# Kernel optimization log

Measured on AMD Instinct MI355X. Metric: run time of the kernel, lower is better.

Reference implementation:

```python
import jax, jax.numpy as jnp
import numpy as np

N, D, IN, HID, OUT, E = 20000, 8, 64, 128, 64, 100000
EPS = 1e-5


def _bn(h, g, b):
    # training-mode BatchNorm1d: biased batch variance, eps=1e-5
    m = h.mean(axis=0)
    v = jnp.mean((h - m) ** 2, axis=0)
    return (h - m) * jax.lax.rsqrt(v + EPS) * g + b


def setup_inputs() -> dict:
    key = jax.random.key(0)
    ks = jax.random.split(key, 12)
    x = jax.random.normal(ks[0], (N, IN), dtype=jnp.float32)
    node_ts = jax.random.uniform(ks[1], (N,), dtype=jnp.float32)
    neighbor_idx = jax.random.randint(ks[2], (N, D), 0, N, dtype=jnp.int32)
    neighbor_ts = jax.random.uniform(ks[3], (N, D), dtype=jnp.float32)
    target = jax.random.randint(ks[4], (2, E), 0, N, dtype=jnp.int32)
    neg_pairs = jax.random.randint(ks[5], (2, E), 0, N, dtype=jnp.int32)
    W1 = jax.random.normal(ks[6], (IN, HID), dtype=jnp.float32) * (1.0 / np.sqrt(IN))
    b1 = jnp.zeros((HID,), jnp.float32)
    g1 = jnp.ones((HID,), jnp.float32)
    be1 = jnp.zeros((HID,), jnp.float32)
    W2 = jax.random.normal(ks[7], (HID, OUT), dtype=jnp.float32) * (1.0 / np.sqrt(HID))
    b2 = jnp.zeros((OUT,), jnp.float32)
    g2 = jnp.ones((OUT,), jnp.float32)
    be2 = jnp.zeros((OUT,), jnp.float32)
    Wd = jax.random.normal(ks[8], (OUT, 1), dtype=jnp.float32) * (1.0 / np.sqrt(OUT))
    bd = jnp.zeros((1,), jnp.float32)
    return {"x": x, "node_ts": node_ts, "neighbor_idx": neighbor_idx,
            "neighbor_ts": neighbor_ts, "target": target, "neg_pairs": neg_pairs,
            "W1": W1, "b1": b1, "g1": g1, "be1": be1,
            "W2": W2, "b2": b2, "g2": g2, "be2": be2, "Wd": Wd, "bd": bd}


def reference(x, node_ts, neighbor_idx, neighbor_ts, target, neg_pairs,
              W1, b1, g1, be1, W2, b2, g2, be2, Wd, bd):
    n = jnp.arange(N, dtype=neighbor_idx.dtype)
    # ---- level-2 queries: every node at its own timestamp ----
    # children = D temporal-neighbor slots + self (self always valid, ts=node_ts)
    c_idx = jnp.concatenate([neighbor_idx, n[:, None]], axis=1)          # [N, D+1]
    c_ts = jnp.concatenate([neighbor_ts, node_ts[:, None]], axis=1)      # [N, D+1]
    mask2 = jnp.concatenate([neighbor_ts <= node_ts[:, None],
                             jnp.ones((N, 1), bool)], axis=1)            # [N, D+1]
    # ---- level-1 queries: each (child node, child ts) pair ----
    ci = c_idx.reshape(-1)                                               # [M]
    cts = c_ts.reshape(-1)
    gc_idx = jnp.concatenate([neighbor_idx[ci], ci[:, None]], axis=1)    # [M, D+1]
    mask1 = jnp.concatenate([neighbor_ts[ci] <= cts[:, None],
                             jnp.ones((ci.shape[0], 1), bool)], axis=1)
    # ---- layer 0: raw features of grandchildren ----
    h0 = x[gc_idx]                                                       # [M, D+1, IN]
    m1 = mask1.astype(x.dtype)
    agg1 = jnp.einsum('mk,mkf->mf', m1, h0) / m1.sum(1, keepdims=True)   # masked mean
    h1 = jax.nn.relu(_bn(agg1 @ W1 + b1, g1, be1))                       # [M, HID]
    h1 = h1.reshape(N, D + 1, HID)
    # ---- layer 2 aggregation over temporal children ----
    m2 = mask2.astype(x.dtype)
    agg2 = jnp.einsum('nk,nkf->nf', m2, h1) / m2.sum(1, keepdims=True)
    embs = jax.nn.relu(_bn(agg2 @ W2 + b2, g2, be2))                     # [N, OUT]
    # ---- HadNet link decoder + BCEWithLogits ----
    pos = (embs[target[0]] * embs[target[1]]) @ Wd + bd                  # [E, 1]
    neg = (embs[neg_pairs[0]] * embs[neg_pairs[1]]) @ Wd + bd            # [E, 1]
    preds = jnp.concatenate([pos, neg], axis=0)[:, 0]                    # [2E]
    labels = jnp.concatenate([jnp.ones((E,), x.dtype), jnp.zeros((E,), x.dtype)])
    loss = jnp.mean(jnp.maximum(preds, 0.0) - preds * labels
                    + jnp.log1p(jnp.exp(-jnp.abs(preds))))
    return loss
```

## Files before the change

### kernel.cpp

```cpp
#include <hip/hip_runtime.h>
#include <math.h>

constexpr int kN = 20000;
constexpr int kD = 8;
constexpr int kE = 100000;
constexpr int kM = kN * 9;
constexpr int kTiles1 = kM / 16;
constexpr int kTilesN = kN / 16;
constexpr float kEps = 1e-5f;

constexpr int S_SUM1 = 0, S_SQ1 = 128, S_SUM2 = 256, S_SQ2 = 320;

constexpr size_t OFF_M     = 0;
constexpr size_t OFF_PRE2  = 23040000;
constexpr size_t OFF_STATS = 28160000;
constexpr size_t OFF_CNT   = OFF_STATS + 1536;
constexpr size_t OFF_RI    = OFF_CNT + 720000;

typedef short short8 __attribute__((ext_vector_type(8)));
typedef float floatx4 __attribute__((ext_vector_type(4)));

__device__ __forceinline__ unsigned f2bf(float f) {
  unsigned u = __float_as_uint(f);
  u += 0x7fffu + ((u >> 16) & 1u);
  return u >> 16;
}

__global__ __launch_bounds__(256) void k0_prefix(
    const float* __restrict__ x, const float* __restrict__ node_ts,
    const int* __restrict__ nidx, const float* __restrict__ nts,
    unsigned short* __restrict__ M, int* __restrict__ rowinfo,
    float* __restrict__ cntf)
{
  int c = blockIdx.x * 4 + (threadIdx.x >> 6);
  const int lane = threadIdx.x & 63;
  c = __builtin_amdgcn_readfirstlane(c);

  float ts[8]; int id[8];
#pragma unroll
  for (int j = 0; j < kD; ++j) { ts[j] = nts[c * kD + j]; id[j] = nidx[c * kD + j]; }

#define CSWAP(A, B)                                                   \
  { float ta = ts[A], tb = ts[B]; int ia = id[A], ib = id[B];         \
    bool sw = tb < ta;                                                \
    ts[A] = sw ? tb : ta; ts[B] = sw ? ta : tb;                       \
    id[A] = sw ? ib : ia; id[B] = sw ? ia : ib; }
  CSWAP(0, 1) CSWAP(2, 3) CSWAP(0, 2) CSWAP(1, 3) CSWAP(1, 2)
  CSWAP(4, 5) CSWAP(6, 7) CSWAP(4, 6) CSWAP(5, 7) CSWAP(5, 6)
  CSWAP(0, 4) CSWAP(1, 5) CSWAP(2, 6) CSWAP(3, 7)
  CSWAP(2, 4) CSWAP(3, 5)
  CSWAP(1, 2) CSWAP(3, 4) CSWAP(5, 6)
#undef CSWAP

  float s = x[c * 64 + lane];
  unsigned short* mp = M + (size_t)c * 9 * 64 + lane;
  mp[0] = (unsigned short)f2bf(s);
#pragma unroll
  for (int r = 1; r <= kD; ++r) {
    s += x[id[r - 1] * 64 + lane];
    mp[r * 64] = (unsigned short)f2bf(s / (float)(r + 1));
  }

  const int m = blockIdx.x * 256 + threadIdx.x;
  if (m < kM) {
    const int n = (int)((unsigned)m / 9u);
    const int slot = m - n * 9;
    int cc; float t;
    if (slot < kD) { cc = nidx[n * kD + slot]; t = nts[n * kD + slot]; }
    else           { cc = n;                   t = node_ts[n]; }
    int rank = 0;
#pragma unroll
    for (int j = 0; j < kD; ++j) rank += (nts[cc * kD + j] <= t) ? 1 : 0;
    rowinfo[m] = cc * 9 + rank;
    atomicAdd(&cntf[cc * 9 + rank], 1.0f);
  }
}

__global__ __launch_bounds__(256, 3) void k1_stats(
    const unsigned short* __restrict__ M, const float* __restrict__ cntf,
    const float* __restrict__ W1, const float* __restrict__ b1,
    float* __restrict__ stats)
{
  __shared__ unsigned short W1T[128 * 72];
  __shared__ float redS[256][8];
  __shared__ float redQ[256][8];

  const int tid = threadIdx.x;
  const int lane = tid & 63;
  const int wave = tid >> 6;
  const int l15 = lane & 15;
  const int q = lane >> 4;

  for (int i = tid; i < 8192; i += 256) {
    int n = i >> 6, k = i & 63;
    W1T[n * 72 + k] = (unsigned short)f2bf(W1[k * 128 + n]);
  }
  __syncthreads();

  short8 bf[8][2];
#pragma unroll
  for (int cc = 0; cc < 8; ++cc)
#pragma unroll
    for (int s = 0; s < 2; ++s)
      bf[cc][s] = *(const short8*)&W1T[(cc * 16 + l15) * 72 + q * 8 + s * 32];

  float b1c[8];
#pragma unroll
  for (int cc = 0; cc < 8; ++cc) b1c[cc] = b1[cc * 16 + l15];

  float sum8[8], sq8[8];
#pragma unroll
  for (int cc = 0; cc < 8; ++cc) { sum8[cc] = 0.f; sq8[cc] = 0.f; }

  const int gw = blockIdx.x * 4 + wave;
  const int nw = gridDim.x * 4;

  for (int t = gw; t < kTiles1; t += nw) {
    const unsigned short* mp = M + (size_t)(t * 16 + l15) * 64;
    short8 af0 = *(const short8*)(mp + q * 8);
    short8 af1 = *(const short8*)(mp + 32 + q * 8);
    float c4[4];
#pragma unroll
    for (int i = 0; i < 4; ++i) c4[i] = cntf[t * 16 + q * 4 + i];

    floatx4 acc[8];
#pragma unroll
    for (int cc = 0; cc < 8; ++cc) {
      acc[cc] = (floatx4){0.f, 0.f, 0.f, 0.f};
      acc[cc] = __builtin_amdgcn_mfma_f32_16x16x32_bf16(af0, bf[cc][0], acc[cc], 0, 0, 0);
      acc[cc] = __builtin_amdgcn_mfma_f32_16x16x32_bf16(af1, bf[cc][1], acc[cc], 0, 0, 0);
    }
#pragma unroll
    for (int cc = 0; cc < 8; ++cc) {
#pragma unroll
      for (int i = 0; i < 4; ++i) {
        float v = acc[cc][i] + b1c[cc];
        sum8[cc] += c4[i] * v;
        sq8[cc]  += c4[i] * v * v;
      }
    }
  }

  __syncthreads();
#pragma unroll
  for (int cc = 0; cc < 8; ++cc) { redS[tid][cc] = sum8[cc]; redQ[tid][cc] = sq8[cc]; }
  __syncthreads();
  if (tid < 128) {
    int cc = tid >> 4, r15 = tid & 15;
    float s = 0.f, qq = 0.f;
#pragma unroll
    for (int w = 0; w < 4; ++w)
#pragma unroll
      for (int p = 0; p < 4; ++p) {
        int T = w * 64 + p * 16 + r15;
        s += redS[T][cc]; qq += redQ[T][cc];
      }
    atomicAdd(&stats[S_SUM1 + tid], s);
    atomicAdd(&stats[S_SQ1 + tid], qq);
  }
}

__global__ __launch_bounds__(256, 2) void k3_fused(
    const unsigned short* __restrict__ M, const int* __restrict__ rowinfo,
    const float* __restrict__ node_ts, const float* __restrict__ nts,
    const float* __restrict__ stats_in, const float* __restrict__ g1,
    const float* __restrict__ be1, const float* __restrict__ W1,
    const float* __restrict__ b1, const float* __restrict__ W2,
    const float* __restrict__ b2, float* __restrict__ stats_out,
    float* __restrict__ pre2)
{
  __shared__ __attribute__((aligned(16))) unsigned short W1T[128 * 72];
  __shared__ __attribute__((aligned(16))) unsigned short W2T[64 * 136];
  __shared__ __attribute__((aligned(16))) unsigned short sm[144 * 132];
  __shared__ __attribute__((aligned(16))) unsigned short aggT[16 * 136];
  __shared__ float sc1[128], sh1[128];
  __shared__ float wlds[144];
  __shared__ float winv[16];

  const int tid = threadIdx.x;
  const int lane = tid & 63;
  const int wave = tid >> 6;
  const int l15 = lane & 15;
  const int q = lane >> 4;

  for (int i = tid; i < 8192; i += 256) {
    int n = i >> 6, k = i & 63;
    W1T[n * 72 + k] = (unsigned short)f2bf(W1[k * 128 + n]);
  }
  for (int i = tid; i < 8192; i += 256) {
    int n = i >> 7, k = i & 127;
    W2T[n * 136 + k] = (unsigned short)f2bf(W2[k * 64 + n]);
  }
  if (tid < 128) {
    float mean = stats_in[S_SUM1 + tid] * (1.f / kM);
    float var  = stats_in[S_SQ1 + tid] * (1.f / kM) - mean * mean;
    float s    = g1[tid] * rsqrtf(var + kEps);
    sc1[tid] = s; sh1[tid] = be1[tid] - mean * s;
  }
  __syncthreads();

  short8 bf[8][2];
  float b1c[8], scc[8], shc[8];
#pragma unroll
  for (int cc = 0; cc < 8; ++cc) {
    int col = cc * 16 + l15;
#pragma unroll
    for (int s = 0; s < 2; ++s)
      bf[cc][s] = *(const short8*)&W1T[col * 72 + q * 8 + s * 32];
    b1c[cc] = b1[col]; scc[cc] = sc1[col]; shc[cc] = sh1[col];
  }
  short8 bfr2[4];
#pragma unroll
  for (int s = 0; s < 4; ++s)
    bfr2[s] = *(const short8*)&W2T[(wave * 16 + l15) * 136 + q * 8 + s * 32];
  const float b2w = b2[wave * 16 + l15];

  float sumS = 0.f, sumQ = 0.f;

  for (int tb = blockIdx.x; tb < kTilesN; tb += gridDim.x) {
    const int node0 = tb * 16;
    const int row0 = tb * 144;

    if (tid < 144) {
      int ln = tid / 9;
      int slot = tid - ln * 9;
      int nn = node0 + ln;
      float w = 1.f;
      if (slot < kD) w = (nts[nn * kD + slot] <= node_ts[nn]) ? 1.f : 0.f;
      wlds[tid] = w;
    }
    __syncthreads();
    if (tid < 16) {
      float swv = 0.f;
#pragma unroll
      for (int r = 0; r < 9; ++r) swv += wlds[tid * 9 + r];
      winv[tid] = 1.f / swv;
    }

    for (int tl = wave; tl < 9; tl += 4) {
      const int ri = rowinfo[row0 + tl * 16 + l15];
      const unsigned short* mp = M + (size_t)ri * 64;
      short8 af0 = *(const short8*)(mp + q * 8);
      short8 af1 = *(const short8*)(mp + 32 + q * 8);
      floatx4 acc[8];
#pragma unroll
      for (int cc = 0; cc < 8; ++cc) {
        acc[cc] = (floatx4){0.f, 0.f, 0.f, 0.f};
        acc[cc] = __builtin_amdgcn_mfma_f32_16x16x32_bf16(af0, bf[cc][0], acc[cc], 0, 0, 0);
        acc[cc] = __builtin_amdgcn_mfma_f32_16x16x32_bf16(af1, bf[cc][1], acc[cc], 0, 0, 0);
      }
#pragma unroll
      for (int cc = 0; cc < 8; ++cc) {
        int col = cc * 16 + l15;
#pragma unroll
        for (int i = 0; i < 4; ++i) {
          float v = acc[cc][i] + b1c[cc];
          float val = fmaxf(fmaf(v, scc[cc], shc[cc]), 0.f);
          int rl = tl * 16 + q * 4 + i;
          val *= wlds[rl];
          sm[rl * 132 + col] = (unsigned short)f2bf(val);
        }
      }
    }
    __syncthreads();

#pragma unroll
    for (int k = 0; k < 4; ++k) {
      int it = tid + k * 256;
      int nd = it >> 6, cp = it & 63;
      float s0 = 0.f, s1 = 0.f;
#pragma unroll
      for (int r = 0; r < 9; ++r) {
        unsigned u = *(const unsigned*)&sm[(nd * 9 + r) * 132 + cp * 2];
        s0 += __uint_as_float(u << 16);
        s1 += __uint_as_float(u & 0xffff0000u);
      }
      float iv = winv[nd];
      *(unsigned*)&aggT[nd * 136 + cp * 2] = f2bf(s0 * iv) | (f2bf(s1 * iv) << 16);
    }
    __syncthreads();

    short8 af2[4];
#pragma unroll
    for (int s = 0; s < 4; ++s)
      af2[s] = *(const short8*)&aggT[l15 * 136 + q * 8 + s * 32];
    floatx4 acc2 = (floatx4){0.f, 0.f, 0.f, 0.f};
#pragma unroll
    for (int s = 0; s < 4; ++s)
      acc2 = __builtin_amdgcn_mfma_f32_16x16x32_bf16(af2[s], bfr2[s], acc2, 0, 0, 0);
#pragma unroll
    for (int i = 0; i < 4; ++i) {
      float v = acc2[i] + b2w;
      int nrow = node0 + q * 4 + i;
      pre2[(size_t)nrow * 64 + wave * 16 + l15] = v;
      sumS += v; sumQ += v * v;
    }
  }

  sumS += __shfl_xor(sumS, 16); sumS += __shfl_xor(sumS, 32);
  sumQ += __shfl_xor(sumQ, 16); sumQ += __shfl_xor(sumQ, 32);
  if (lane < 16) {
    atomicAdd(&stats_out[S_SUM2 + wave * 16 + lane], sumS);
    atomicAdd(&stats_out[S_SQ2 + wave * 16 + lane], sumQ);
  }
}

__global__ __launch_bounds__(256) void k6_loss(
    const float* __restrict__ pre2, const float* __restrict__ stats,
    const float* __restrict__ g2, const float* __restrict__ be2,
    const float* __restrict__ Wd, const int* __restrict__ tgt,
    const int* __restrict__ neg, const float* __restrict__ bd,
    float* __restrict__ out)
{
  __shared__ float scl[64], shl[64], wdl[64];
  __shared__ float redl[256];
  const int tid = threadIdx.x;
  if (tid < 64) {
    float mean = stats[S_SUM2 + tid] * (1.f / kN);
    float var  = stats[S_SQ2 + tid] * (1.f / kN) - mean * mean;
    float s    = g2[tid] * rsqrtf(var + kEps);
    scl[tid] = s; shl[tid] = be2[tid] - mean * s; wdl[tid] = Wd[tid];
  }
  __syncthreads();

  const int tq = tid & 15;
  const int qb = tid >> 4;
  const int c0 = tq * 4;
  const float4 sc4 = {scl[c0], scl[c0 + 1], scl[c0 + 2], scl[c0 + 3]};
  const float4 sh4 = {shl[c0], shl[c0 + 1], shl[c0 + 2], shl[c0 + 3]};
  const float4 wd4 = {wdl[c0], wdl[c0 + 1], wdl[c0 + 2], wdl[c0 + 3]};
  const float bd0 = bd[0];

  float lsum = 0.f;
  const int e0 = blockIdx.x * 128 + qb * 8;
#pragma unroll
  for (int it = 0; it < 8; ++it) {
    int e = e0 + it;
    if (e < 2 * kE) {
      int i, j; float lab;
      if (e < kE) { i = tgt[e];      j = tgt[kE + e]; lab = 1.f; }
      else        { i = neg[e - kE]; j = neg[e];      lab = 0.f; }
      float4 a = *(const float4*)(pre2 + (size_t)i * 64 + c0);
      float4 b = *(const float4*)(pre2 + (size_t)j * 64 + c0);
      float eix = fmaxf(fmaf(a.x, sc4.x, sh4.x), 0.f) * wd4.x;
      float eiy = fmaxf(fmaf(a.y, sc4.y, sh4.y), 0.f) * wd4.y;
      float eiz = fmaxf(fmaf(a.z, sc4.z, sh4.z), 0.f) * wd4.z;
      float eiw = fmaxf(fmaf(a.w, sc4.w, sh4.w), 0.f) * wd4.w;
      float ejx = fmaxf(fmaf(b.x, sc4.x, sh4.x), 0.f);
      float ejy = fmaxf(fmaf(b.y, sc4.y, sh4.y), 0.f);
      float ejz = fmaxf(fmaf(b.z, sc4.z, sh4.z), 0.f);
      float ejw = fmaxf(fmaf(b.w, sc4.w, sh4.w), 0.f);
      float p = eix * ejx + eiy * ejy + eiz * ejz + eiw * ejw;
      p += __shfl_xor(p, 1); p += __shfl_xor(p, 2);
      p += __shfl_xor(p, 4); p += __shfl_xor(p, 8);
      p += bd0;
      float l = fmaxf(p, 0.f) - p * lab + log1pf(expf(-fabsf(p)));
      if (tq == 0) lsum += l;
    }
  }
  redl[tid] = lsum;
  __syncthreads();
  for (int s = 128; s > 0; s >>= 1) {
    if (tid < s) redl[tid] += redl[tid + s];
    __syncthreads();
  }
  if (tid == 0) atomicAdd(out, redl[0] * (1.f / (2 * kE)));
}

extern "C" void kernel_launch(void* const* d_in, const int* in_sizes, int n_in,
                              void* d_out, int out_size, void* d_ws, size_t ws_size,
                              hipStream_t stream) {
  (void)in_sizes; (void)n_in; (void)out_size; (void)ws_size;
  const float* x       = (const float*)d_in[0];
  const float* node_ts = (const float*)d_in[1];
  const int*   nidx    = (const int*)d_in[2];
  const float* nts     = (const float*)d_in[3];
  const int*   tgt     = (const int*)d_in[4];
  const int*   neg     = (const int*)d_in[5];
  const float* W1      = (const float*)d_in[6];
  const float* b1      = (const float*)d_in[7];
  const float* g1      = (const float*)d_in[8];
  const float* be1     = (const float*)d_in[9];
  const float* W2      = (const float*)d_in[10];
  const float* b2      = (const float*)d_in[11];
  const float* g2      = (const float*)d_in[12];
  const float* be2     = (const float*)d_in[13];
  const float* Wd      = (const float*)d_in[14];
  const float* bd      = (const float*)d_in[15];

  char* ws = (char*)d_ws;
  unsigned short* Mbuf = (unsigned short*)(ws + OFF_M);
  float* pre2  = (float*)(ws + OFF_PRE2);
  float* stats = (float*)(ws + OFF_STATS);
  float* cntf  = (float*)(ws + OFF_CNT);
  int*   rinfo = (int*)(ws + OFF_RI);
  float* out   = (float*)d_out;

  hipMemsetAsync(stats, 0, 1536 + 720000, stream);
  hipMemsetAsync(out, 0, sizeof(float), stream);

  k0_prefix<<<kN / 4, 256, 0, stream>>>(x, node_ts, nidx, nts, Mbuf, rinfo, cntf);
  k1_stats<<<704, 256, 0, stream>>>(Mbuf, cntf, W1, b1, stats);
  k3_fused<<<512, 256, 0, stream>>>(Mbuf, rinfo, node_ts, nts, stats, g1, be1,
                                    W1, b1, W2, b2, stats, pre2);
  k6_loss<<<(2 * kE + 127) / 128, 256, 0, stream>>>(pre2, stats, g2, be2, Wd,
                                                    tgt, neg, bd, out);
}
```

Baseline: 207.1 us.

## Fuse all stages into one persistent kernel with software grid barriers

Merges the four kernel launches into one persistent kernel of 512 blocks. Stages are separated by atomic-counter grid barriers, and the W1/W2 bf16 transposes are staged once per block instead of once per kernel. It also adds a pass that writes post-BN2 embeddings as bf16, so the loss stage gathers half the bytes and skips the per-edge BN math. This removes launch gaps and redundant weight setup, but adds five grid-wide spin barriers, relies on all 512 blocks being co-resident, and lowers embedding precision to bf16.

Measured after the change: 440.4 us. 2.13x slower.

```diff
diff --git a/kernel.cpp b/kernel.cpp
--- a/kernel.cpp
+++ b/kernel.cpp
@@ -8,14 +8,18 @@
 constexpr int kTiles1 = kM / 16;
 constexpr int kTilesN = kN / 16;
 constexpr float kEps = 1e-5f;
+constexpr int kGrid = 512;
+constexpr int kThreads = 256;
 
 constexpr int S_SUM1 = 0, S_SQ1 = 128, S_SUM2 = 256, S_SQ2 = 320;
 
 constexpr size_t OFF_M     = 0;
 constexpr size_t OFF_PRE2  = 23040000;
-constexpr size_t OFF_STATS = 28160000;
-constexpr size_t OFF_CNT   = OFF_STATS + 1536;
-constexpr size_t OFF_RI    = OFF_CNT + 720000;
+constexpr size_t OFF_EMBS  = 28160000;
+constexpr size_t OFF_STATS = 30720000;
+constexpr size_t OFF_CNT   = 30721536;
+constexpr size_t OFF_RI    = 31441536;
+constexpr size_t OFF_BAR   = 32161536;
 
 typedef short short8 __attribute__((ext_vector_type(8)));
 typedef float floatx4 __attribute__((ext_vector_type(4)));
@@ -26,43 +30,96 @@
   return u >> 16;
 }
 
-__global__ __launch_bounds__(256) void k0_prefix(
+__device__ __forceinline__ void grid_bar(int* bar, int target) {
+  __syncthreads();
+  if (threadIdx.x == 0) {
+    __threadfence();
+    __hip_atomic_fetch_add(bar, 1, __ATOMIC_RELEASE, __HIP_MEMORY_SCOPE_AGENT);
+    while (__hip_atomic_load(bar, __ATOMIC_RELAXED, __HIP_MEMORY_SCOPE_AGENT) < target)
+      __builtin_amdgcn_s_sleep(2);
+    __threadfence();
+  }
+  __syncthreads();
+}
+
+constexpr int kLdsBytes = 43008;
+
+__global__ __launch_bounds__(kThreads, 2) void k_all(
     const float* __restrict__ x, const float* __restrict__ node_ts,
     const int* __restrict__ nidx, const float* __restrict__ nts,
-    unsigned short* __restrict__ M, int* __restrict__ rowinfo,
-    float* __restrict__ cntf)
+    const int* __restrict__ tgt, const int* __restrict__ neg,
+    const float* __restrict__ W1, const float* __restrict__ b1,
+    const float* __restrict__ g1, const float* __restrict__ be1,
+    const float* __restrict__ W2, const float* __restrict__ b2,
+    const float* __restrict__ g2, const float* __restrict__ be2,
+    const float* __restrict__ Wd, const float* __restrict__ bd,
+    unsigned short* __restrict__ Mb, float* __restrict__ pre2,
+    unsigned short* __restrict__ embs, float* __restrict__ stats,
+    float* __restrict__ cntf, int* __restrict__ rowinfo,
+    int* bar, float* out)
 {
-  int c = blockIdx.x * 4 + (threadIdx.x >> 6);
-  const int lane = threadIdx.x & 63;
-  c = __builtin_amdgcn_readfirstlane(c);
-
-  float ts[8]; int id[8];
-#pragma unroll
-  for (int j = 0; j < kD; ++j) { ts[j] = nts[c * kD + j]; id[j] = nidx[c * kD + j]; }
-
+  __shared__ __attribute__((aligned(16))) char ldsb[kLdsBytes];
+
+  const int tid = threadIdx.x;
+  const int lane = tid & 63;
+  const int wave = tid >> 6;
+  const int l15 = lane & 15;
+  const int q = lane >> 4;
+  const int gw = blockIdx.x * 4 + wave;
+
+  unsigned short* W1T = (unsigned short*)ldsb;
+  unsigned short* W2T = (unsigned short*)(ldsb + 18432);
+
+  for (int i = tid; i < 8192; i += 256) {
+    int nn = i >> 6, k = i & 63;
+    W1T[nn * 72 + k] = (unsigned short)f2bf(W1[k * 128 + nn]);
+  }
+  for (int i = tid; i < 8192; i += 256) {
+    int nn = i >> 7, k = i & 127;
+    W2T[nn * 136 + k] = (unsigned short)f2bf(W2[k * 64 + nn]);
+  }
+  if (blockIdx.x == 0 && tid == 0) *out = 0.f;
+  __syncthreads();
+
+  short8 bf[8][2];
+  float b1c[8];
+#pragma unroll
+  for (int cc = 0; cc < 8; ++cc) {
+    int col = cc * 16 + l15;
+#pragma unroll
+    for (int s = 0; s < 2; ++s)
+      bf[cc][s] = *(const short8*)&W1T[col * 72 + q * 8 + s * 32];
+    b1c[cc] = b1[col];
+  }
+
+  grid_bar(bar, 1 * kGrid);
+
+  for (int c0 = gw; c0 < kN; c0 += kGrid * 4) {
+    const int c = __builtin_amdgcn_readfirstlane(c0);
+    float ts[8]; int id[8];
+#pragma unroll
+    for (int j = 0; j < kD; ++j) { ts[j] = nts[c * kD + j]; id[j] = nidx[c * kD + j]; }
 #define CSWAP(A, B)                                                   \
-  { float ta = ts[A], tb = ts[B]; int ia = id[A], ib = id[B];         \
-    bool sw = tb < ta;                                                \
-    ts[A] = sw ? tb : ta; ts[B] = sw ? ta : tb;                       \
-    id[A] = sw ? ib : ia; id[B] = sw ? ia : ib; }
-  CSWAP(0, 1) CSWAP(2, 3) CSWAP(0, 2) CSWAP(1, 3) CSWAP(1, 2)
-  CSWAP(4, 5) CSWAP(6, 7) CSWAP(4, 6) CSWAP(5, 7) CSWAP(5, 6)
-  CSWAP(0, 4) CSWAP(1, 5) CSWAP(2, 6) CSWAP(3, 7)
-  CSWAP(2, 4) CSWAP(3, 5)
-  CSWAP(1, 2) CSWAP(3, 4) CSWAP(5, 6)
+    { float ta = ts[A], tb = ts[B]; int ia = id[A], ib = id[B];       \
+      bool sw = tb < ta;                                              \
+      ts[A] = sw ? tb : ta; ts[B] = sw ? ta : tb;                     \
+      id[A] = sw ? ib : ia; id[B] = sw ? ia : ib; }
+    CSWAP(0, 1) CSWAP(2, 3) CSWAP(0, 2) CSWAP(1, 3) CSWAP(1, 2)
+    CSWAP(4, 5) CSWAP(6, 7) CSWAP(4, 6) CSWAP(5, 7) CSWAP(5, 6)
+    CSWAP(0, 4) CSWAP(1, 5) CSWAP(2, 6) CSWAP(3, 7)
+    CSWAP(2, 4) CSWAP(3, 5)
+    CSWAP(1, 2) CSWAP(3, 4) CSWAP(5, 6)
 #undef CSWAP
-
-  float s = x[c * 64 + lane];
-  unsigned short* mp = M + (size_t)c * 9 * 64 + lane;
-  mp[0] = (unsigned short)f2bf(s);
-#pragma unroll
-  for (int r = 1; r <= kD; ++r) {
-    s += x[id[r - 1] * 64 + lane];
-    mp[r * 64] = (unsigned short)f2bf(s / (float)(r + 1));
-  }
-
-  const int m = blockIdx.x * 256 + threadIdx.x;
-  if (m < kM) {
+    float s = x[c * 64 + lane];
+    unsigned short* mp = Mb + (size_t)c * 9 * 64 + lane;
+    mp[0] = (unsigned short)f2bf(s);
+#pragma unroll
+    for (int r = 1; r <= kD; ++r) {
+      s += x[id[r - 1] * 64 + lane];
+      mp[r * 64] = (unsigned short)f2bf(s / (float)(r + 1));
+    }
+  }
+  for (int m = blockIdx.x * 256 + tid; m < kM; m += kGrid * 256) {
     const int n = (int)((unsigned)m / 9u);
     const int slot = m - n * 9;
     int cc; float t;
@@ -74,174 +131,22 @@
     rowinfo[m] = cc * 9 + rank;
     atomicAdd(&cntf[cc * 9 + rank], 1.0f);
   }
-}
-
-__global__ __launch_bounds__(256, 3) void k1_stats(
-    const unsigned short* __restrict__ M, const float* __restrict__ cntf,
-    const float* __restrict__ W1, const float* __restrict__ b1,
-    float* __restrict__ stats)
-{
-  __shared__ unsigned short W1T[128 * 72];
-  __shared__ float redS[256][8];
-  __shared__ float redQ[256][8];
-
-  const int tid = threadIdx.x;
-  const int lane = tid & 63;
-  const int wave = tid >> 6;
-  const int l15 = lane & 15;
-  const int q = lane >> 4;
-
-  for (int i = tid; i < 8192; i += 256) {
-    int n = i >> 6, k = i & 63;
-    W1T[n * 72 + k] = (unsigned short)f2bf(W1[k * 128 + n]);
-  }
-  __syncthreads();
-
-  short8 bf[8][2];
-#pragma unroll
-  for (int cc = 0; cc < 8; ++cc)
-#pragma unroll
-    for (int s = 0; s < 2; ++s)
-      bf[cc][s] = *(const short8*)&W1T[(cc * 16 + l15) * 72 + q * 8 + s * 32];
-
-  float b1c[8];
-#pragma unroll
-  for (int cc = 0; cc < 8; ++cc) b1c[cc] = b1[cc * 16 + l15];
-
-  float sum8[8], sq8[8];
-#pragma unroll
-  for (int cc = 0; cc < 8; ++cc) { sum8[cc] = 0.f; sq8[cc] = 0.f; }
-
-  const int gw = blockIdx.x * 4 + wave;
-  const int nw = gridDim.x * 4;
-
-  for (int t = gw; t < kTiles1; t += nw) {
-    const unsigned short* mp = M + (size_t)(t * 16 + l15) * 64;
-    short8 af0 = *(const short8*)(mp + q * 8);
-    short8 af1 = *(const short8*)(mp + 32 + q * 8);
-    float c4[4];
-#pragma unroll
-    for (int i = 0; i < 4; ++i) c4[i] = cntf[t * 16 + q * 4 + i];
-
-    floatx4 acc[8];
-#pragma unroll
-    for (int cc = 0; cc < 8; ++cc) {
-      acc[cc] = (floatx4){0.f, 0.f, 0.f, 0.f};
-      acc[cc] = __builtin_amdgcn_mfma_f32_16x16x32_bf16(af0, bf[cc][0], acc[cc], 0, 0, 0);
-      acc[cc] = __builtin_amdgcn_mfma_f32_16x16x32_bf16(af1, bf[cc][1], acc[cc], 0, 0, 0);
-    }
-#pragma unroll
-    for (int cc = 0; cc < 8; ++cc) {
-#pragma unroll
-      for (int i = 0; i < 4; ++i) {
-        float v = acc[cc][i] + b1c[cc];
-        sum8[cc] += c4[i] * v;
-        sq8[cc]  += c4[i] * v * v;
-      }
-    }
-  }
-
-  __syncthreads();
-#pragma unroll
-  for (int cc = 0; cc < 8; ++cc) { redS[tid][cc] = sum8[cc]; redQ[tid][cc] = sq8[cc]; }
-  __syncthreads();
-  if (tid < 128) {
-    int cc = tid >> 4, r15 = tid & 15;
-    float s = 0.f, qq = 0.f;
-#pragma unroll
-    for (int w = 0; w < 4; ++w)
-#pragma unroll
-      for (int p = 0; p < 4; ++p) {
-        int T = w * 64 + p * 16 + r15;
-        s += redS[T][cc]; qq += redQ[T][cc];
-      }
-    atomicAdd(&stats[S_SUM1 + tid], s);
-    atomicAdd(&stats[S_SQ1 + tid], qq);
-  }
-}
-
-__global__ __launch_bounds__(256, 2) void k3_fused(
-    const unsigned short* __restrict__ M, const int* __restrict__ rowinfo,
-    const float* __restrict__ node_ts, const float* __restrict__ nts,
-    const float* __restrict__ stats_in, const float* __restrict__ g1,
-    const float* __restrict__ be1, const float* __restrict__ W1,
-    const float* __restrict__ b1, const float* __restrict__ W2,
-    const float* __restrict__ b2, float* __restrict__ stats_out,
-    float* __restrict__ pre2)
-{
-  __shared__ __attribute__((aligned(16))) unsigned short W1T[128 * 72];
-  __shared__ __attribute__((aligned(16))) unsigned short W2T[64 * 136];
-  __shared__ __attribute__((aligned(16))) unsigned short sm[144 * 132];
-  __shared__ __attribute__((aligned(16))) unsigned short aggT[16 * 136];
-  __shared__ float sc1[128], sh1[128];
-  __shared__ float wlds[144];
-  __shared__ float winv[16];
-
-  const int tid = threadIdx.x;
-  const int lane = tid & 63;
-  const int wave = tid >> 6;
-  const int l15 = lane & 15;
-  const int q = lane >> 4;
-
-  for (int i = tid; i < 8192; i += 256) {
-    int n = i >> 6, k = i & 63;
-    W1T[n * 72 + k] = (unsigned short)f2bf(W1[k * 128 + n]);
-  }
-  for (int i = tid; i < 8192; i += 256) {
-    int n = i >> 7, k = i & 127;
-    W2T[n * 136 + k] = (unsigned short)f2bf(W2[k * 64 + n]);
-  }
-  if (tid < 128) {
-    float mean = stats_in[S_SUM1 + tid] * (1.f / kM);
-    float var  = stats_in[S_SQ1 + tid] * (1.f / kM) - mean * mean;
-    float s    = g1[tid] * rsqrtf(var + kEps);
-    sc1[tid] = s; sh1[tid] = be1[tid] - mean * s;
-  }
-  __syncthreads();
-
-  short8 bf[8][2];
-  float b1c[8], scc[8], shc[8];
-#pragma unroll
-  for (int cc = 0; cc < 8; ++cc) {
-    int col = cc * 16 + l15;
-#pragma unroll
-    for (int s = 0; s < 2; ++s)
-      bf[cc][s] = *(const short8*)&W1T[col * 72 + q * 8 + s * 32];
-    b1c[cc] = b1[col]; scc[cc] = sc1[col]; shc[cc] = sh1[col];
-  }
-  short8 bfr2[4];
-#pragma unroll
-  for (int s = 0; s < 4; ++s)
-    bfr2[s] = *(const short8*)&W2T[(wave * 16 + l15) * 136 + q * 8 + s * 32];
-  const float b2w = b2[wave * 16 + l15];
-
-  float sumS = 0.f, sumQ = 0.f;
-
-  for (int tb = blockIdx.x; tb < kTilesN; tb += gridDim.x) {
-    const int node0 = tb * 16;
-    const int row0 = tb * 144;
-
-    if (tid < 144) {
-      int ln = tid / 9;
-      int slot = tid - ln * 9;
-      int nn = node0 + ln;
-      float w = 1.f;
-      if (slot < kD) w = (nts[nn * kD + slot] <= node_ts[nn]) ? 1.f : 0.f;
-      wlds[tid] = w;
-    }
-    __syncthreads();
-    if (tid < 16) {
-      float swv = 0.f;
-#pragma unroll
-      for (int r = 0; r < 9; ++r) swv += wlds[tid * 9 + r];
-      winv[tid] = 1.f / swv;
-    }
-
-    for (int tl = wave; tl < 9; tl += 4) {
-      const int ri = rowinfo[row0 + tl * 16 + l15];
-      const unsigned short* mp = M + (size_t)ri * 64;
+
+  grid_bar(bar, 2 * kGrid);
+
+  {
+    float sum8[8], sq8[8];
+#pragma unroll
+    for (int cc = 0; cc < 8; ++cc) { sum8[cc] = 0.f; sq8[cc] = 0.f; }
+
+    for (int t = gw; t < kTiles1; t += kGrid * 4) {
+      const unsigned short* mp = Mb + (size_t)(t * 16 + l15) * 64;
       short8 af0 = *(const short8*)(mp + q * 8);
       short8 af1 = *(const short8*)(mp + 32 + q * 8);
+      float c4[4];
+#pragma unroll
+      for (int i = 0; i < 4; ++i) c4[i] = cntf[t * 16 + q * 4 + i];
+
       floatx4 acc[8];
 #pragma unroll
       for (int cc = 0; cc < 8; ++cc) {
@@ -251,120 +156,216 @@
       }
 #pragma unroll
       for (int cc = 0; cc < 8; ++cc) {
-        int col = cc * 16 + l15;
 #pragma unroll
         for (int i = 0; i < 4; ++i) {
           float v = acc[cc][i] + b1c[cc];
-          float val = fmaxf(fmaf(v, scc[cc], shc[cc]), 0.f);
-          int rl = tl * 16 + q * 4 + i;
-          val *= wlds[rl];
-          sm[rl * 132 + col] = (unsigned short)f2bf(val);
-        }
-      }
-    }
+          sum8[cc] += c4[i] * v;
+          sq8[cc]  += c4[i] * v * v;
+        }
+      }
+    }
+
     __syncthreads();
-
-#pragma unroll
-    for (int k = 0; k < 4; ++k) {
-      int it = tid + k * 256;
-      int nd = it >> 6, cp = it & 63;
-      float s0 = 0.f, s1 = 0.f;
-#pragma unroll
-      for (int r = 0; r < 9; ++r) {
-        unsigned u = *(const unsigned*)&sm[(nd * 9 + r) * 132 + cp * 2];
-        s0 += __uint_as_float(u << 16);
-        s1 += __uint_as_float(u & 0xffff0000u);
-      }
-      float iv = winv[nd];
-      *(unsigned*)&aggT[nd * 136 + cp * 2] = f2bf(s0 * iv) | (f2bf(s1 * iv) << 16);
-    }
+    float* redS = (float*)ldsb;
+    float* redQ = (float*)(ldsb + 8192);
+#pragma unroll
+    for (int cc = 0; cc < 8; ++cc) { redS[tid * 8 + cc] = sum8[cc]; redQ[tid * 8 + cc] = sq8[cc]; }
     __syncthreads();
-
-    short8 af2[4];
+    if (tid < 128) {
+      int cc = tid >> 4, r15 = tid & 15;
+      float s = 0.f, qq = 0.f;
+#pragma unroll
+      for (int w = 0; w < 4; ++w)
+#pragma unroll
+        for (int p = 0; p < 4; ++p) {
+          int T = w * 64 + p * 16 + r15;
+          s += redS[T * 8 + cc]; qq += redQ[T * 8 + cc];
+        }
+      atomicAdd(&stats[S_SUM1 + tid], s);
+      atomicAdd(&stats[S_SQ1 + tid], qq);
+    }
+  }
+
+  grid_bar(bar, 3 * kGrid);
+
+  {
+    unsigned short* sm   = (unsigned short*)ldsb;
+    unsigned short* aggT = (unsigned short*)(ldsb + 38016);
+    float* wlds = (float*)(ldsb + 42368);
+    float* winv = (float*)(ldsb + 42944);
+
+    short8 bfr2[4];
 #pragma unroll
     for (int s = 0; s < 4; ++s)
-      af2[s] = *(const short8*)&aggT[l15 * 136 + q * 8 + s * 32];
-    floatx4 acc2 = (floatx4){0.f, 0.f, 0.f, 0.f};
-#pragma unroll
-    for (int s = 0; s < 4; ++s)
-      acc2 = __builtin_amdgcn_mfma_f32_16x16x32_bf16(af2[s], bfr2[s], acc2, 0, 0, 0);
-#pragma unroll
-    for (int i = 0; i < 4; ++i) {
-      float v = acc2[i] + b2w;
-      int nrow = node0 + q * 4 + i;
-      pre2[(size_t)nrow * 64 + wave * 16 + l15] = v;
-      sumS += v; sumQ += v * v;
-    }
-  }
-
-  sumS += __shfl_xor(sumS, 16); sumS += __shfl_xor(sumS, 32);
-  sumQ += __shfl_xor(sumQ, 16); sumQ += __shfl_xor(sumQ, 32);
-  if (lane < 16) {
-    atomicAdd(&stats_out[S_SUM2 + wave * 16 + lane], sumS);
-    atomicAdd(&stats_out[S_SQ2 + wave * 16 + lane], sumQ);
-  }
-}
-
-__global__ __launch_bounds__(256) void k6_loss(
-    const float* __restrict__ pre2, const float* __restrict__ stats,
-    const float* __restrict__ g2, const float* __restrict__ be2,
-    const float* __restrict__ Wd, const int* __restrict__ tgt,
-    const int* __restrict__ neg, const float* __restrict__ bd,
-    float* __restrict__ out)
-{
-  __shared__ float scl[64], shl[64], wdl[64];
-  __shared__ float redl[256];
-  const int tid = threadIdx.x;
-  if (tid < 64) {
-    float mean = stats[S_SUM2 + tid] * (1.f / kN);
-    float var  = stats[S_SQ2 + tid] * (1.f / kN) - mean * mean;
-    float s    = g2[tid] * rsqrtf(var + kEps);
-    scl[tid] = s; shl[tid] = be2[tid] - mean * s; wdl[tid] = Wd[tid];
-  }
-  __syncthreads();
-
-  const int tq = tid & 15;
-  const int qb = tid >> 4;
-  const int c0 = tq * 4;
-  const float4 sc4 = {scl[c0], scl[c0 + 1], scl[c0 + 2], scl[c0 + 3]};
-  const float4 sh4 = {shl[c0], shl[c0 + 1], shl[c0 + 2], shl[c0 + 3]};
-  const float4 wd4 = {wdl[c0], wdl[c0 + 1], wdl[c0 + 2], wdl[c0 + 3]};
-  const float bd0 = bd[0];
-
-  float lsum = 0.f;
-  const int e0 = blockIdx.x * 128 + qb * 8;
-#pragma unroll
-  for (int it = 0; it < 8; ++it) {
-    int e = e0 + it;
-    if (e < 2 * kE) {
-      int i, j; float lab;
-      if (e < kE) { i = tgt[e];      j = tgt[kE + e]; lab = 1.f; }
-      else        { i = neg[e - kE]; j = neg[e];      lab = 0.f; }
-      float4 a = *(const float4*)(pre2 + (size_t)i * 64 + c0);
-      float4 b = *(const float4*)(pre2 + (size_t)j * 64 + c0);
-      float eix = fmaxf(fmaf(a.x, sc4.x, sh4.x), 0.f) * wd4.x;
-      float eiy = fmaxf(fmaf(a.y, sc4.y, sh4.y), 0.f) * wd4.y;
-      float eiz = fmaxf(fmaf(a.z, sc4.z, sh4.z), 0.f) * wd4.z;
-      float eiw = fmaxf(fmaf(a.w, sc4.w, sh4.w), 0.f) * wd4.w;
-      float ejx = fmaxf(fmaf(b.x, sc4.x, sh4.x), 0.f);
-      float ejy = fmaxf(fmaf(b.y, sc4.y, sh4.y), 0.f);
-      float ejz = fmaxf(fmaf(b.z, sc4.z, sh4.z), 0.f);
-      float ejw = fmaxf(fmaf(b.w, sc4.w, sh4.w), 0.f);
-      float p = eix * ejx + eiy * ejy + eiz * ejz + eiw * ejw;
-      p += __shfl_xor(p, 1); p += __shfl_xor(p, 2);
-      p += __shfl_xor(p, 4); p += __shfl_xor(p, 8);
-      p += bd0;
-      float l = fmaxf(p, 0.f) - p * lab + log1pf(expf(-fabsf(p)));
-      if (tq == 0) lsum += l;
-    }
-  }
-  redl[tid] = lsum;
-  __syncthreads();
-  for (int s = 128; s > 0; s >>= 1) {
-    if (tid < s) redl[tid] += redl[tid + s];
+      bfr2[s] = *(const short8*)&W2T[(wave * 16 + l15) * 136 + q * 8 + s * 32];
+    const float b2w = b2[wave * 16 + l15];
+    float scc[8], shc[8];
+#pragma unroll
+    for (int cc = 0; cc < 8; ++cc) {
+      int col = cc * 16 + l15;
+      float mean = stats[S_SUM1 + col] * (1.f / kM);
+      float var  = stats[S_SQ1 + col] * (1.f / kM) - mean * mean;
+      float s    = g1[col] * rsqrtf(var + kEps);
+      scc[cc] = s; shc[cc] = be1[col] - mean * s;
+    }
+
+    float sumS = 0.f, sumQ = 0.f;
+
+    for (int tb = blockIdx.x; tb < kTilesN; tb += kGrid) {
+      const int node0 = tb * 16;
+      const int row0 = tb * 144;
+
+      if (tid < 144) {
+        int ln = tid / 9;
+        int slot = tid - ln * 9;
+        int nn = node0 + ln;
+        float w = 1.f;
+        if (slot < kD) w = (nts[nn * kD + slot] <= node_ts[nn]) ? 1.f : 0.f;
+        wlds[tid] = w;
+      }
+      __syncthreads();
+      if (tid < 16) {
+        float swv = 0.f;
+#pragma unroll
+        for (int r = 0; r < 9; ++r) swv += wlds[tid * 9 + r];
+        winv[tid] = 1.f / swv;
+      }
+
+      for (int tl = wave; tl < 9; tl += 4) {
+        const int ri = rowinfo[row0 + tl * 16 + l15];
+        const unsigned short* mp = Mb + (size_t)ri * 64;
+        short8 af0 = *(const short8*)(mp + q * 8);
+        short8 af1 = *(const short8*)(mp + 32 + q * 8);
+        floatx4 acc[8];
+#pragma unroll
+        for (int cc = 0; cc < 8; ++cc) {
+          acc[cc] = (floatx4){0.f, 0.f, 0.f, 0.f};
+          acc[cc] = __builtin_amdgcn_mfma_f32_16x16x32_bf16(af0, bf[cc][0], acc[cc], 0, 0, 0);
+          acc[cc] = __builtin_amdgcn_mfma_f32_16x16x32_bf16(af1, bf[cc][1], acc[cc], 0, 0, 0);
+        }
+        float w4[4];
+#pragma unroll
+        for (int i = 0; i < 4; ++i) w4[i] = wlds[tl * 16 + q * 4 + i];
+#pragma unroll
+        for (int cc = 0; cc < 8; ++cc) {
+          int col = cc * 16 + l15;
+#pragma unroll
+          for (int i = 0; i < 4; ++i) {
+            float v = acc[cc][i] + b1c[cc];
+            float val = fmaxf(fmaf(v, scc[cc], shc[cc]), 0.f) * w4[i];
+            sm[(tl * 16 + q * 4 + i) * 132 + col] = (unsigned short)f2bf(val);
+          }
+        }
+      }
+      __syncthreads();
+
+#pragma unroll
+      for (int k = 0; k < 4; ++k) {
+        int it = tid + k * 256;
+        int nd = it >> 6, cp = it & 63;
+        float s0 = 0.f, s1 = 0.f;
+#pragma unroll
+        for (int r = 0; r < 9; ++r) {
+          unsigned u = *(const unsigned*)&sm[(nd * 9 + r) * 132 + cp * 2];
+          s0 += __uint_as_float(u << 16);
+          s1 += __uint_as_float(u & 0xffff0000u);
+        }
+        float iv = winv[nd];
+        *(unsigned*)&aggT[nd * 136 + cp * 2] = f2bf(s0 * iv) | (f2bf(s1 * iv) << 16);
+      }
+      __syncthreads();
+
+      short8 af2[4];
+#pragma unroll
+      for (int s = 0; s < 4; ++s)
+        af2[s] = *(const short8*)&aggT[l15 * 136 + q * 8 + s * 32];
+      floatx4 acc2 = (floatx4){0.f, 0.f, 0.f, 0.f};
+#pragma unroll
+      for (int s = 0; s < 4; ++s)
+        acc2 = __builtin_amdgcn_mfma_f32_16x16x32_bf16(af2[s], bfr2[s], acc2, 0, 0, 0);
+#pragma unroll
+      for (int i = 0; i < 4; ++i) {
+        float v = acc2[i] + b2w;
+        int nrow = node0 + q * 4 + i;
+        pre2[(size_t)nrow * 64 + wave * 16 + l15] = v;
+        sumS += v; sumQ += v * v;
+      }
+    }
+
+    sumS += __shfl_xor(sumS, 16); sumS += __shfl_xor(sumS, 32);
+    sumQ += __shfl_xor(sumQ, 16); sumQ += __shfl_xor(sumQ, 32);
+    if (lane < 16) {
+      atomicAdd(&stats[S_SUM2 + wave * 16 + lane], sumS);
+      atomicAdd(&stats[S_SQ2 + wave * 16 + lane], sumQ);
+    }
+  }
+
+  grid_bar(bar, 4 * kGrid);
+
+  {
+    const int gid = blockIdx.x * 256 + tid;
+    const int cp = gid & 31;
+    const int c0 = 2 * cp;
+    float m0 = stats[S_SUM2 + c0] * (1.f / kN);
+    float v0 = stats[S_SQ2 + c0] * (1.f / kN) - m0 * m0;
+    float s0 = g2[c0] * rsqrtf(v0 + kEps);
+    float h0 = be2[c0] - m0 * s0;
+    float m1 = stats[S_SUM2 + c0 + 1] * (1.f / kN);
+    float v1 = stats[S_SQ2 + c0 + 1] * (1.f / kN) - m1 * m1;
+    float s1 = g2[c0 + 1] * rsqrtf(v1 + kEps);
+    float h1 = be2[c0 + 1] - m1 * s1;
+    unsigned* edw = (unsigned*)embs;
+    for (int i = gid; i < kN * 32; i += kGrid * 256) {
+      float2 p = *(const float2*)(pre2 + (size_t)i * 2);
+      unsigned lo = f2bf(fmaxf(fmaf(p.x, s0, h0), 0.f));
+      unsigned hi = f2bf(fmaxf(fmaf(p.y, s1, h1), 0.f));
+      edw[i] = lo | (hi << 16);
+    }
+  }
+
+  grid_bar(bar, 5 * kGrid);
+
+  {
+    const int tq = tid & 15;
+    const int qb = tid >> 4;
+    const int c0 = tq * 4;
+    const float4 wd4 = {Wd[c0], Wd[c0 + 1], Wd[c0 + 2], Wd[c0 + 3]};
+    const float bd0 = bd[0];
+    float lsum = 0.f;
+    for (int vb = blockIdx.x; vb < (2 * kE + 127) / 128; vb += kGrid) {
+      const int e0 = vb * 128 + qb * 8;
+#pragma unroll
+      for (int it = 0; it < 8; ++it) {
+        int e = e0 + it;
+        if (e < 2 * kE) {
+          int i, j; float lab;
+          if (e < kE) { i = tgt[e];      j = tgt[kE + e]; lab = 1.f; }
+          else        { i = neg[e - kE]; j = neg[e];      lab = 0.f; }
+          uint2 ua = *(const uint2*)&embs[(size_t)i * 64 + c0];
+          uint2 ub = *(const uint2*)&embs[(size_t)j * 64 + c0];
+          float a0 = __uint_as_float(ua.x << 16),        a1 = __uint_as_float(ua.x & 0xffff0000u);
+          float a2 = __uint_as_float(ua.y << 16),        a3 = __uint_as_float(ua.y & 0xffff0000u);
+          float e0v = __uint_as_float(ub.x << 16),       e1v = __uint_as_float(ub.x & 0xffff0000u);
+          float e2v = __uint_as_float(ub.y << 16),       e3v = __uint_as_float(ub.y & 0xffff0000u);
+          float p = (a0 * wd4.x) * e0v + (a1 * wd4.y) * e1v
+                  + (a2 * wd4.z) * e2v + (a3 * wd4.w) * e3v;
+          p += __shfl_xor(p, 1); p += __shfl_xor(p, 2);
+          p += __shfl_xor(p, 4); p += __shfl_xor(p, 8);
+          p += bd0;
+          float l = fmaxf(p, 0.f) - p * lab + log1pf(expf(-fabsf(p)));
+          if (tq == 0) lsum += l;
+        }
+      }
+    }
+    float* redl = (float*)ldsb;
+    redl[tid] = lsum;
     __syncthreads();
-  }
-  if (tid == 0) atomicAdd(out, redl[0] * (1.f / (2 * kE)));
+    for (int s = 128; s > 0; s >>= 1) {
+      if (tid < s) redl[tid] += redl[tid + s];
+      __syncthreads();
+    }
+    if (tid == 0) atomicAdd(out, redl[0] * (1.f / (2 * kE)));
+  }
 }
 
 extern "C" void kernel_launch(void* const* d_in, const int* in_sizes, int n_in,
@@ -391,18 +392,16 @@
   char* ws = (char*)d_ws;
   unsigned short* Mbuf = (unsigned short*)(ws + OFF_M);
   float* pre2  = (float*)(ws + OFF_PRE2);
+  unsigned short* embs = (unsigned short*)(ws + OFF_EMBS);
   float* stats = (float*)(ws + OFF_STATS);
   float* cntf  = (float*)(ws + OFF_CNT);
   int*   rinfo = (int*)(ws + OFF_RI);
+  int*   bar   = (int*)(ws + OFF_BAR);
   float* out   = (float*)d_out;
 
-  hipMemsetAsync(stats, 0, 1536 + 720000, stream);
-  hipMemsetAsync(out, 0, sizeof(float), stream);
-
-  k0_prefix<<<kN / 4, 256, 0, stream>>>(x, node_ts, nidx, nts, Mbuf, rinfo, cntf);
-  k1_stats<<<704, 256, 0, stream>>>(Mbuf, cntf, W1, b1, stats);
-  k3_fused<<<512, 256, 0, stream>>>(Mbuf, rinfo, node_ts, nts, stats, g1, be1,
-                                    W1, b1, W2, b2, stats, pre2);
-  k6_loss<<<(2 * kE + 127) / 128, 256, 0, stream>>>(pre2, stats, g2, be2, Wd,
-                                                    tgt, neg, bd, out);
+  hipMemsetAsync(ws + OFF_STATS, 0, (OFF_BAR + 64) - OFF_STATS, stream);
+
+  k_all<<<kGrid, kThreads, 0, stream>>>(
+      x, node_ts, nidx, nts, tgt, neg, W1, b1, g1, be1, W2, b2, g2, be2,
+      Wd, bd, Mbuf, pre2, embs, stats, cntf, rinfo, bar, out);
 }
```
